# Kernel tuning notes

Measured on AMD Instinct MI355X. Metric: run time of the kernel, lower is better.

Reference implementation:

```python
import jax, jax.numpy as jnp
import numpy as np

N_EMBD = 1024
N_HEAD = 16
HEAD_SIZE = N_EMBD // N_HEAD


def setup_inputs() -> dict:
    key = jax.random.key(0)
    k_x, k_w, k_b = jax.random.split(key, 3)
    B, T, C = 2, 2048, N_EMBD
    x = jax.random.normal(k_x, (B, T, C), dtype=jnp.float32)
    # Linear(n_embd, 3*n_embd): weight [C, 3C] (applied as x @ W), bias [3C]
    w_qkv = jax.random.normal(k_w, (C, 3 * C), dtype=jnp.float32) * (1.0 / np.sqrt(C))
    b_qkv = jax.random.normal(k_b, (3 * C,), dtype=jnp.float32) * 0.02
    return {"x": x, "w_qkv": w_qkv, "b_qkv": b_qkv}


def reference(x, w_qkv, b_qkv):
    B, T, C = x.shape
    H, D = N_HEAD, HEAD_SIZE
    qkv = x @ w_qkv + b_qkv                      # [B, T, 3C]
    q, k, v = jnp.split(qkv, 3, axis=-1)         # each [B, T, C]
    # [B, T, C] -> [B, H, T, D]
    q = q.reshape(B, T, H, D).transpose(0, 2, 1, 3)
    k = k.reshape(B, T, H, D).transpose(0, 2, 1, 3)
    v = v.reshape(B, T, H, D).transpose(0, 2, 1, 3)
    scores = jnp.einsum('bhqd,bhkd->bhqk', q, k) / jnp.sqrt(jnp.float32(D))
    causal = jnp.tril(jnp.ones((T, T), dtype=bool))  # allow j <= i
    scores = jnp.where(causal[None, None, :, :], scores, -jnp.inf)
    weights = jax.nn.softmax(scores, axis=-1)    # [B, H, T, T]
    out = jnp.einsum('bhqk,bhkd->bhqd', weights, v)
    out = out.transpose(0, 2, 1, 3).reshape(B, T, C)
    return out
```

## Files before the change

kernel.cpp:

```cpp
#include <hip/hip_runtime.h>
#include <hip/hip_bf16.h>


#define CDIM  1024
#define C3    3072
#define HS    64
#define TLEN  2048
#define KVT   128
#define KSTR  72
#define VSTR  136
#define SCL   0.1803368801111204f

typedef __attribute__((ext_vector_type(8))) short bf16x8;
typedef __attribute__((ext_vector_type(4))) float f32x4;
typedef __attribute__((ext_vector_type(4))) unsigned short u16x4;

__device__ __forceinline__ unsigned short f2b(float f) {
    unsigned u = __float_as_uint(f);
    unsigned r = (u + 0x7FFFu + ((u >> 16) & 1u)) >> 16;
    return (unsigned short)r;
}
__device__ __forceinline__ float b2f(unsigned short u) {
    return __uint_as_float(((unsigned)u) << 16);
}
__device__ __forceinline__ float fexp2(float x) {
    return __builtin_amdgcn_exp2f(x);
}
__device__ __forceinline__ unsigned pkbf(float a, float b) {
    float2 f; f.x = a; f.y = b;
    __hip_bfloat162 h = __float22bfloat162_rn(f);
    union { __hip_bfloat162 h2; unsigned u; } c;
    c.h2 = h;
    return c.u;
}
__device__ __forceinline__ void gl_lds16(const unsigned short* g, unsigned short* l) {
    __builtin_amdgcn_global_load_lds((const __attribute__((address_space(1))) void*)g,
                                     (__attribute__((address_space(3))) void*)l, 16, 0, 0);
}
__device__ __forceinline__ int detect_bf(const void* bias, int lane) {
    unsigned w = ((const unsigned*)bias)[lane];
    unsigned e = (w >> 7) & 0xFF;
    unsigned long long m = __ballot(e >= 100 && e <= 135);
    return __popcll(m) >= 48;
}

__device__ __forceinline__ void plswap(unsigned x, unsigned& y0, unsigned& y1) {
    unsigned aa = x, bb = x;
    asm("v_permlane32_swap_b32 %0, %1" : "+v"(aa), "+v"(bb));
    asm("v_permlane16_swap_b32 %0, %1" : "+v"(aa), "+v"(bb));
    y0 = aa; y1 = bb;
}
__device__ __forceinline__ bf16x8 xfrag(unsigned x00, unsigned x01,
                                        unsigned x10, unsigned x11, int qsel) {
    unsigned y000, y100, y001, y101, y010, y110, y011, y111;
    plswap(x00, y000, y100);
    plswap(x01, y001, y101);
    plswap(x10, y010, y110);
    plswap(x11, y011, y111);
    union { unsigned u[4]; bf16x8 v; } r;
    r.u[0] = qsel ? y010 : y000;
    r.u[1] = qsel ? y011 : y001;
    r.u[2] = qsel ? y110 : y100;
    r.u[3] = qsel ? y111 : y101;
    return r.v;
}

__global__ __launch_bounds__(256) void k_prep(const void* __restrict__ w,
                                              const void* __restrict__ x,
                                              const void* __restrict__ bias,
                                              unsigned short* __restrict__ wt,
                                              unsigned short* __restrict__ xb) {
    __shared__ unsigned short tile[64 * 66];
    int t = threadIdx.x;
    int isbf = detect_bf(bias, t & 63);
    int bid = blockIdx.x;

    if (bid < 768) {
        int n0 = (bid % 48) * 64;
        int k0 = (bid / 48) * 64;
        for (int i = 0; i < 16; ++i) {
            int idx = t + i * 256;
            int r = idx >> 6, c = idx & 63;
            unsigned short v;
            if (isbf) v = ((const unsigned short*)w)[(k0 + r) * C3 + n0 + c];
            else      v = f2b(((const float*)w)[(k0 + r) * C3 + n0 + c]);
            tile[r * 66 + c] = v;
        }
        __syncthreads();
        for (int i = 0; i < 16; ++i) {
            int idx = t + i * 256;
            int r = idx >> 6, c = idx & 63;
            wt[(n0 + r) * CDIM + k0 + c] = tile[c * 66 + r];
        }
    }
    if (!isbf) {
        const float* s = (const float*)x;
        unsigned* d = (unsigned*)xb;
        int base = bid * 1024;
        for (int j = t; j < 1024; j += 256) {
            int idx = base + j;
            float a = s[2 * idx], b = s[2 * idx + 1];
            d[idx] = (unsigned)f2b(a) | ((unsigned)f2b(b) << 16);
        }
    }
}

__global__ __launch_bounds__(256, 3) void k_gemm_qkv(const void* __restrict__ xraw,
                                                     const unsigned short* __restrict__ xb,
                                                     const void* __restrict__ biasraw,
                                                     const unsigned short* __restrict__ Bt,
                                                     unsigned short* __restrict__ qk,
                                                     unsigned short* __restrict__ vtg) {
    __shared__ __align__(16) unsigned short As[128 * 64];
    __shared__ __align__(16) unsigned short Bs[128 * 64];
    int tid  = threadIdx.x;
    int lane = tid & 63, wv = tid >> 6;
    int quad = lane >> 4, l16 = lane & 15;
    int isbf = detect_bf(biasraw, lane);
    const unsigned short* A = isbf ? (const unsigned short*)xraw : xb;

    int m0 = blockIdx.y * 128, n0 = blockIdx.x * 128;
    int wm = (wv >> 1) * 64, wn = (wv & 1) * 64;

    f32x4 acc[4][4] = {};

    int srow = wv * 8 + (lane >> 3);
    int kcg8 = (((lane & 7) ^ (lane >> 3)) * 8);
    const unsigned short* Ag = A  + (m0 + srow) * CDIM + kcg8;
    const unsigned short* Bg = Bt + (n0 + srow) * CDIM + kcg8;
    unsigned short* lA = &As[srow * 64 + (lane & 7) * 8];
    unsigned short* lB = &Bs[srow * 64 + (lane & 7) * 8];

    for (int k0 = 0; k0 < CDIM; k0 += 64) {
        __syncthreads();
        for (int j = 0; j < 4; ++j) {
            gl_lds16(Ag + j * (32 * CDIM), lA + j * (32 * 64));
            gl_lds16(Bg + j * (32 * CDIM), lB + j * (32 * 64));
        }
        Ag += 64; Bg += 64;
        __syncthreads();

        for (int kk = 0; kk < 2; ++kk) {
            int sw = (l16 & 7);
            bf16x8 af[4], bfr[4];
            for (int mt = 0; mt < 4; ++mt)
                af[mt] = *(const bf16x8*)&As[(wm + mt * 16 + l16) * 64 + (((kk * 4 + quad) ^ sw) * 8)];
            for (int nt = 0; nt < 4; ++nt)
                bfr[nt] = *(const bf16x8*)&Bs[(wn + nt * 16 + l16) * 64 + (((kk * 4 + quad) ^ sw) * 8)];
            for (int mt = 0; mt < 4; ++mt)
                for (int nt = 0; nt < 4; ++nt)
                    acc[mt][nt] = __builtin_amdgcn_mfma_f32_16x16x32_bf16(af[mt], bfr[nt], acc[mt][nt], 0, 0, 0);
        }
    }

    if (n0 < 2048) {
        for (int mt = 0; mt < 4; ++mt) {
            int row = m0 + wm + mt * 16 + quad * 4;
            for (int nt = 0; nt < 4; ++nt) {
                int col = n0 + wn + nt * 16 + l16;
                float bv = isbf ? b2f(((const unsigned short*)biasraw)[col])
                                : ((const float*)biasraw)[col];
                for (int i = 0; i < 4; ++i)
                    qk[(row + i) * 2048 + col] = f2b(acc[mt][nt][i] + bv);
            }
        }
    } else {
        for (int mt = 0; mt < 4; ++mt) {
            int row = m0 + wm + mt * 16 + quad * 4;
            int t = row & 2047, b = row >> 11;
            for (int nt = 0; nt < 4; ++nt) {
                int col = n0 + wn + nt * 16 + l16;
                float bv = isbf ? b2f(((const unsigned short*)biasraw)[col])
                                : ((const float*)biasraw)[col];
                int hh = (col - 2048) >> 6, d = (col - 2048) & 63;
                u16x4 pk;
                for (int i = 0; i < 4; ++i) pk[i] = f2b(acc[mt][nt][i] + bv);
                *(u16x4*)&vtg[((b * 16 + hh) * 64 + d) * TLEN + t] = pk;
            }
        }
    }
}

__global__ __launch_bounds__(512, 4) void k_attn(const unsigned short* __restrict__ qk,
                                                 const unsigned short* __restrict__ vtg,
                                                 const void* __restrict__ biasraw,
                                                 void* __restrict__ outv) {
    __shared__ __align__(16) unsigned short Ks[2][128 * KSTR];
    __shared__ __align__(16) unsigned short Vt[2][64 * VSTR];

    int tid  = threadIdx.x;
    int lane = tid & 63, wv = tid >> 6;
    int quad = lane >> 4, l16 = lane & 15;
    int isbf = detect_bf(biasraw, lane);
    int bh = blockIdx.x;
    int y  = blockIdx.y;
    int jj = (y < 8) ? (15 - 2 * y) : (2 * (y - 8));
    int b = bh >> 4, h = bh & 15;
    int rowbase = b * TLEN;

    int qt = 8 * jj + wv;
    int q0 = qt * 16;
    int T  = jj + 1;

    bf16x8 qf[2];
    for (int kh = 0; kh < 2; ++kh)
        qf[kh] = *(const bf16x8*)&qk[(rowbase + q0 + l16) * 2048 + h * HS + kh * 32 + quad * 8];

    f32x4 o[4] = {};
    float ls = 0.f;

    int krow = tid >> 3;
    int kc8  = (tid & 7) * 8;
    int vrow = tid >> 4;
    int vc8  = (tid & 15) * 8;
    const unsigned short* kgB = qk  + (rowbase + krow) * 2048 + CDIM + h * HS + kc8;
    const unsigned short* vgB = vtg + (bh * 64 + vrow) * TLEN + vc8;

    {
        uint4 k0 = *(const uint4*)kgB;
        uint4 k1 = *(const uint4*)(kgB + 64 * 2048);
        uint4 v0 = *(const uint4*)vgB;
        uint4 v1 = *(const uint4*)(vgB + 32 * TLEN);
        *(uint4*)&Ks[0][krow * KSTR + kc8]        = k0;
        *(uint4*)&Ks[0][(krow + 64) * KSTR + kc8] = k1;
        *(uint4*)&Vt[0][vrow * VSTR + vc8]        = v0;
        *(uint4*)&Vt[0][(vrow + 32) * VSTR + vc8] = v1;
    }
    __syncthreads();

    for (int t = 0; t < T; ++t) {
        int cur = t & 1;
        const unsigned short* KsC = Ks[cur];
        const unsigned short* VtC = Vt[cur];
        int kv0 = t * KVT;

        uint4 kn0, kn1, vn0, vn1;
        bool pf = (t + 1 < T);
        if (pf) {
            const unsigned short* kg = kgB + (t + 1) * KVT * 2048;
            const unsigned short* vg = vgB + (t + 1) * KVT;
            kn0 = *(const uint4*)kg;
            kn1 = *(const uint4*)(kg + 64 * 2048);
            vn0 = *(const uint4*)vg;
            vn1 = *(const uint4*)(vg + 32 * TLEN);
        }

        f32x4 s[8];
        #pragma unroll
        for (int nt = 0; nt < 8; ++nt) {
            bf16x8 kf0 = *(const bf16x8*)&KsC[(nt * 16 + l16) * KSTR + quad * 8];
            bf16x8 kf1 = *(const bf16x8*)&KsC[(nt * 16 + l16) * KSTR + 32 + quad * 8];
            f32x4 z = {};
            z = __builtin_amdgcn_mfma_f32_16x16x32_bf16(kf0, qf[0], z, 0, 0, 0);
            z = __builtin_amdgcn_mfma_f32_16x16x32_bf16(kf1, qf[1], z, 0, 0, 0);
            s[nt] = z;
        }

        unsigned sp[8][2];
        float psum = 0.f;
        if (t == T - 1) {
            int q = q0 + l16;
            #pragma unroll
            for (int nt = 0; nt < 8; ++nt) {
                float p[4];
                #pragma unroll
                for (int i = 0; i < 4; ++i) {
                    float arg = fminf(fmaf(s[nt][i], SCL, -12.0f), 30.0f);
                    int kv = kv0 + nt * 16 + quad * 4 + i;
                    if (kv > q) arg = -1e30f;
                    p[i] = fexp2(arg);
                    psum += p[i];
                }
                sp[nt][0] = pkbf(p[0], p[1]);
                sp[nt][1] = pkbf(p[2], p[3]);
            }
        } else {
            #pragma unroll
            for (int nt = 0; nt < 8; ++nt) {
                float p[4];
                #pragma unroll
                for (int i = 0; i < 4; ++i) {
                    float arg = fminf(fmaf(s[nt][i], SCL, -12.0f), 30.0f);
                    p[i] = fexp2(arg);
                    psum += p[i];
                }
                sp[nt][0] = pkbf(p[0], p[1]);
                sp[nt][1] = pkbf(p[2], p[3]);
            }
        }
        ls += psum;

        if (pf) {
            int nxt = cur ^ 1;
            *(uint4*)&Ks[nxt][krow * KSTR + kc8]        = kn0;
            *(uint4*)&Ks[nxt][(krow + 64) * KSTR + kc8] = kn1;
            *(uint4*)&Vt[nxt][vrow * VSTR + vc8]        = vn0;
            *(uint4*)&Vt[nxt][(vrow + 32) * VSTR + vc8] = vn1;
        }

        int qsel = quad & 2;
        #pragma unroll
        for (int kq = 0; kq < 4; ++kq) {
            bf16x8 fB = xfrag(sp[2 * kq][0], sp[2 * kq][1],
                              sp[2 * kq + 1][0], sp[2 * kq + 1][1], qsel);
            __builtin_amdgcn_s_setprio(1);
            #pragma unroll
            for (int dt = 0; dt < 4; ++dt) {
                bf16x8 av = *(const bf16x8*)&VtC[(dt * 16 + l16) * VSTR + kq * 32 + quad * 8];
                o[dt] = __builtin_amdgcn_mfma_f32_16x16x32_bf16(av, fB, o[dt], 0, 0, 0);
            }
            __builtin_amdgcn_s_setprio(0);
        }

        __syncthreads();
    }

    {
        float l = ls;
        l += __shfl_xor(l, 16);
        l += __shfl_xor(l, 32);
        float inv = 1.0f / l;
        int q = q0 + l16;
        if (isbf) {
            unsigned short* out = (unsigned short*)outv;
            for (int dt = 0; dt < 4; ++dt) {
                u16x4 ov;
                for (int i = 0; i < 4; ++i) ov[i] = f2b(o[dt][i] * inv);
                *(u16x4*)&out[(rowbase + q) * CDIM + h * HS + dt * 16 + quad * 4] = ov;
            }
        } else {
            float* out = (float*)outv;
            for (int dt = 0; dt < 4; ++dt) {
                float4 ov;
                ov.x = o[dt][0] * inv; ov.y = o[dt][1] * inv;
                ov.z = o[dt][2] * inv; ov.w = o[dt][3] * inv;
                *(float4*)&out[(rowbase + q) * CDIM + h * HS + dt * 16 + quad * 4] = ov;
            }
        }
    }
}

extern "C" void kernel_launch(void* const* d_in, const int* in_sizes, int n_in,
                              void* d_out, int out_size, void* d_ws, size_t ws_size,
                              hipStream_t stream) {
    const void* x    = d_in[0];
    const void* w    = d_in[1];
    const void* bias = d_in[2];

    char* ws = (char*)d_ws;
    unsigned short* xb  = (unsigned short*)ws;
    unsigned short* wt  = (unsigned short*)(ws + (8u  << 20));
    unsigned short* qk  = (unsigned short*)(ws + (16u << 20));
    unsigned short* vtg = (unsigned short*)(ws + (32u << 20));

    k_prep<<<2048, 256, 0, stream>>>(w, x, bias, wt, xb);
    k_gemm_qkv<<<dim3(24, 32), 256, 0, stream>>>(x, xb, bias, wt, qk, vtg);
    k_attn<<<dim3(32, 16), 512, 0, stream>>>(qk, vtg, bias, d_out);
}
```

Measured before the change: 162.9 us.

## Restructure attention into 64-query blocks with split-KV warps and LDS merge

The attention kernel now uses 256-thread blocks, each covering 64 query rows with 64-row KV tiles, and the grid doubles to 32x32. The four warps form two query pairs: each warp handles 32 queries against half of every KV tile, and the partial outputs and row sums are combined through shared memory at the end. The aim is finer-grained blocks for better load balance and occupancy, with causal masking applied only on the diagonal tile and fully masked half-tiles skipped. In exchange there are more KV tile iterations with a barrier each, a merge step, and some warps sitting idle on the final tile.

```diff
diff --git a/kernel.cpp b/kernel.cpp
--- a/kernel.cpp
+++ b/kernel.cpp
@@ -6,9 +6,9 @@
 #define C3    3072
 #define HS    64
 #define TLEN  2048
-#define KVT   128
+#define KVT   64
 #define KSTR  72
-#define VSTR  136
+#define VSTR  72
 #define SCL   0.1803368801111204f
 
 typedef __attribute__((ext_vector_type(8))) short bf16x8;
@@ -181,11 +181,11 @@
     }
 }
 
-__global__ __launch_bounds__(512, 4) void k_attn(const unsigned short* __restrict__ qk,
+__global__ __launch_bounds__(256, 4) void k_attn(const unsigned short* __restrict__ qk,
                                                  const unsigned short* __restrict__ vtg,
                                                  const void* __restrict__ biasraw,
                                                  void* __restrict__ outv) {
-    __shared__ __align__(16) unsigned short Ks[2][128 * KSTR];
+    __shared__ __align__(16) unsigned short Ks[2][64 * KSTR];
     __shared__ __align__(16) unsigned short Vt[2][64 * VSTR];
 
     int tid  = threadIdx.x;
@@ -193,38 +193,38 @@
     int quad = lane >> 4, l16 = lane & 15;
     int isbf = detect_bf(biasraw, lane);
     int bh = blockIdx.x;
-    int y  = blockIdx.y;
-    int jj = (y < 8) ? (15 - 2 * y) : (2 * (y - 8));
+    int g  = 31 - blockIdx.y;
     int b = bh >> 4, h = bh & 15;
     int rowbase = b * TLEN;
 
-    int qt = 8 * jj + wv;
-    int q0 = qt * 16;
-    int T  = jj + 1;
-
-    bf16x8 qf[2];
-    for (int kh = 0; kh < 2; ++kh)
-        qf[kh] = *(const bf16x8*)&qk[(rowbase + q0 + l16) * 2048 + h * HS + kh * 32 + quad * 8];
-
-    f32x4 o[4] = {};
-    float ls = 0.f;
-
-    int krow = tid >> 3;
-    int kc8  = (tid & 7) * 8;
-    int vrow = tid >> 4;
-    int vc8  = (tid & 15) * 8;
-    const unsigned short* kgB = qk  + (rowbase + krow) * 2048 + CDIM + h * HS + kc8;
-    const unsigned short* vgB = vtg + (bh * 64 + vrow) * TLEN + vc8;
+    int s_ = wv >> 1;
+    int p  = wv & 1;
+    int qbase = 64 * g + 32 * s_;
+    int T = g + 1;
+
+    bf16x8 qf[2][2];
+    for (int qt = 0; qt < 2; ++qt)
+        for (int kh = 0; kh < 2; ++kh)
+            qf[qt][kh] = *(const bf16x8*)&qk[(rowbase + qbase + qt * 16 + l16) * 2048
+                                            + h * HS + kh * 32 + quad * 8];
+
+    f32x4 o[2][4] = {};
+    float ls[2] = {0.f, 0.f};
+
+    int srow = tid >> 2;
+    int sc   = (tid & 3) * 8;
+    const unsigned short* kgB = qk  + (rowbase + srow) * 2048 + CDIM + h * HS + sc;
+    const unsigned short* vgB = vtg + (bh * 64 + srow) * TLEN + sc;
 
     {
         uint4 k0 = *(const uint4*)kgB;
-        uint4 k1 = *(const uint4*)(kgB + 64 * 2048);
+        uint4 k1 = *(const uint4*)(kgB + 32);
         uint4 v0 = *(const uint4*)vgB;
-        uint4 v1 = *(const uint4*)(vgB + 32 * TLEN);
-        *(uint4*)&Ks[0][krow * KSTR + kc8]        = k0;
-        *(uint4*)&Ks[0][(krow + 64) * KSTR + kc8] = k1;
-        *(uint4*)&Vt[0][vrow * VSTR + vc8]        = v0;
-        *(uint4*)&Vt[0][(vrow + 32) * VSTR + vc8] = v1;
+        uint4 v1 = *(const uint4*)(vgB + 32);
+        *(uint4*)&Ks[0][srow * KSTR + sc]      = k0;
+        *(uint4*)&Ks[0][srow * KSTR + sc + 32] = k1;
+        *(uint4*)&Vt[0][srow * VSTR + sc]      = v0;
+        *(uint4*)&Vt[0][srow * VSTR + sc + 32] = v1;
     }
     __syncthreads();
 
@@ -233,6 +233,8 @@
         const unsigned short* KsC = Ks[cur];
         const unsigned short* VtC = Vt[cur];
         int kv0 = t * KVT;
+        bool act = (p == 0) || (s_ == 1) || (t < T - 1);
+        bool dm  = (t == T - 1) && (p == s_);
 
         uint4 kn0, kn1, vn0, vn1;
         bool pf = (t + 1 < T);
@@ -240,101 +242,129 @@
             const unsigned short* kg = kgB + (t + 1) * KVT * 2048;
             const unsigned short* vg = vgB + (t + 1) * KVT;
             kn0 = *(const uint4*)kg;
-            kn1 = *(const uint4*)(kg + 64 * 2048);
+            kn1 = *(const uint4*)(kg + 32);
             vn0 = *(const uint4*)vg;
-            vn1 = *(const uint4*)(vg + 32 * TLEN);
-        }
-
-        f32x4 s[8];
-        #pragma unroll
-        for (int nt = 0; nt < 8; ++nt) {
-            bf16x8 kf0 = *(const bf16x8*)&KsC[(nt * 16 + l16) * KSTR + quad * 8];
-            bf16x8 kf1 = *(const bf16x8*)&KsC[(nt * 16 + l16) * KSTR + 32 + quad * 8];
-            f32x4 z = {};
-            z = __builtin_amdgcn_mfma_f32_16x16x32_bf16(kf0, qf[0], z, 0, 0, 0);
-            z = __builtin_amdgcn_mfma_f32_16x16x32_bf16(kf1, qf[1], z, 0, 0, 0);
-            s[nt] = z;
-        }
-
-        unsigned sp[8][2];
-        float psum = 0.f;
-        if (t == T - 1) {
-            int q = q0 + l16;
-            #pragma unroll
-            for (int nt = 0; nt < 8; ++nt) {
-                float p[4];
+            vn1 = *(const uint4*)(vg + 32);
+        }
+
+        unsigned sp[2][2][2];
+        if (act) {
+            bf16x8 kf[2][2];
+            #pragma unroll
+            for (int nt = 0; nt < 2; ++nt) {
+                const unsigned short* kb = &KsC[(32 * p + nt * 16 + l16) * KSTR + quad * 8];
+                kf[nt][0] = *(const bf16x8*)kb;
+                kf[nt][1] = *(const bf16x8*)(kb + 32);
+            }
+            f32x4 sv[2][2];
+            __builtin_amdgcn_s_setprio(1);
+            #pragma unroll
+            for (int qt = 0; qt < 2; ++qt)
                 #pragma unroll
-                for (int i = 0; i < 4; ++i) {
-                    float arg = fminf(fmaf(s[nt][i], SCL, -12.0f), 30.0f);
-                    int kv = kv0 + nt * 16 + quad * 4 + i;
-                    if (kv > q) arg = -1e30f;
-                    p[i] = fexp2(arg);
-                    psum += p[i];
+                for (int nt = 0; nt < 2; ++nt) {
+                    f32x4 z = {};
+                    z = __builtin_amdgcn_mfma_f32_16x16x32_bf16(kf[nt][0], qf[qt][0], z, 0, 0, 0);
+                    z = __builtin_amdgcn_mfma_f32_16x16x32_bf16(kf[nt][1], qf[qt][1], z, 0, 0, 0);
+                    sv[qt][nt] = z;
                 }
-                sp[nt][0] = pkbf(p[0], p[1]);
-                sp[nt][1] = pkbf(p[2], p[3]);
-            }
-        } else {
-            #pragma unroll
-            for (int nt = 0; nt < 8; ++nt) {
-                float p[4];
+            __builtin_amdgcn_s_setprio(0);
+            #pragma unroll
+            for (int qt = 0; qt < 2; ++qt) {
+                float psum = 0.f;
+                int q = qbase + qt * 16 + l16;
                 #pragma unroll
-                for (int i = 0; i < 4; ++i) {
-                    float arg = fminf(fmaf(s[nt][i], SCL, -12.0f), 30.0f);
-                    p[i] = fexp2(arg);
-                    psum += p[i];
+                for (int nt = 0; nt < 2; ++nt) {
+                    float pv[4];
+                    #pragma unroll
+                    for (int i = 0; i < 4; ++i) {
+                        float arg = fminf(fmaf(sv[qt][nt][i], SCL, -12.0f), 30.0f);
+                        if (dm) {
+                            int kv = kv0 + 32 * p + nt * 16 + quad * 4 + i;
+                            if (kv > q) arg = -1e30f;
+                        }
+                        pv[i] = fexp2(arg);
+                        psum += pv[i];
+                    }
+                    sp[qt][nt][0] = pkbf(pv[0], pv[1]);
+                    sp[qt][nt][1] = pkbf(pv[2], pv[3]);
                 }
-                sp[nt][0] = pkbf(p[0], p[1]);
-                sp[nt][1] = pkbf(p[2], p[3]);
-            }
-        }
-        ls += psum;
+                ls[qt] += psum;
+            }
+        }
 
         if (pf) {
             int nxt = cur ^ 1;
-            *(uint4*)&Ks[nxt][krow * KSTR + kc8]        = kn0;
-            *(uint4*)&Ks[nxt][(krow + 64) * KSTR + kc8] = kn1;
-            *(uint4*)&Vt[nxt][vrow * VSTR + vc8]        = vn0;
-            *(uint4*)&Vt[nxt][(vrow + 32) * VSTR + vc8] = vn1;
-        }
-
-        int qsel = quad & 2;
+            *(uint4*)&Ks[nxt][srow * KSTR + sc]      = kn0;
+            *(uint4*)&Ks[nxt][srow * KSTR + sc + 32] = kn1;
+            *(uint4*)&Vt[nxt][srow * VSTR + sc]      = vn0;
+            *(uint4*)&Vt[nxt][srow * VSTR + sc + 32] = vn1;
+        }
+
+        if (act) {
+            int qsel = quad & 2;
+            bf16x8 f0 = xfrag(sp[0][0][0], sp[0][0][1], sp[0][1][0], sp[0][1][1], qsel);
+            bf16x8 f1 = xfrag(sp[1][0][0], sp[1][0][1], sp[1][1][0], sp[1][1][1], qsel);
+            __builtin_amdgcn_s_setprio(1);
+            #pragma unroll
+            for (int dt = 0; dt < 4; ++dt) {
+                bf16x8 av = *(const bf16x8*)&VtC[(dt * 16 + l16) * VSTR + 32 * p + quad * 8];
+                o[0][dt] = __builtin_amdgcn_mfma_f32_16x16x32_bf16(av, f0, o[0][dt], 0, 0, 0);
+                o[1][dt] = __builtin_amdgcn_mfma_f32_16x16x32_bf16(av, f1, o[1][dt], 0, 0, 0);
+            }
+            __builtin_amdgcn_s_setprio(0);
+        }
+
+        __syncthreads();
+    }
+
+    #pragma unroll
+    for (int qt = 0; qt < 2; ++qt) {
+        ls[qt] += __shfl_xor(ls[qt], 16);
+        ls[qt] += __shfl_xor(ls[qt], 32);
+    }
+    float* mrg  = (float*)&Ks[0][0];
+    float* lbuf = (float*)&Vt[0][0];
+
+    if (p == 1) {
         #pragma unroll
-        for (int kq = 0; kq < 4; ++kq) {
-            bf16x8 fB = xfrag(sp[2 * kq][0], sp[2 * kq][1],
-                              sp[2 * kq + 1][0], sp[2 * kq + 1][1], qsel);
-            __builtin_amdgcn_s_setprio(1);
-            #pragma unroll
-            for (int dt = 0; dt < 4; ++dt) {
-                bf16x8 av = *(const bf16x8*)&VtC[(dt * 16 + l16) * VSTR + kq * 32 + quad * 8];
-                o[dt] = __builtin_amdgcn_mfma_f32_16x16x32_bf16(av, fB, o[dt], 0, 0, 0);
-            }
-            __builtin_amdgcn_s_setprio(0);
-        }
-
-        __syncthreads();
-    }
-
-    {
-        float l = ls;
-        l += __shfl_xor(l, 16);
-        l += __shfl_xor(l, 32);
-        float inv = 1.0f / l;
-        int q = q0 + l16;
-        if (isbf) {
-            unsigned short* out = (unsigned short*)outv;
-            for (int dt = 0; dt < 4; ++dt) {
-                u16x4 ov;
-                for (int i = 0; i < 4; ++i) ov[i] = f2b(o[dt][i] * inv);
-                *(u16x4*)&out[(rowbase + q) * CDIM + h * HS + dt * 16 + quad * 4] = ov;
-            }
-        } else {
-            float* out = (float*)outv;
-            for (int dt = 0; dt < 4; ++dt) {
-                float4 ov;
-                ov.x = o[dt][0] * inv; ov.y = o[dt][1] * inv;
-                ov.z = o[dt][2] * inv; ov.w = o[dt][3] * inv;
-                *(float4*)&out[(rowbase + q) * CDIM + h * HS + dt * 16 + quad * 4] = ov;
+        for (int qt = 0; qt < 2; ++qt)
+            #pragma unroll
+            for (int dt = 0; dt < 4; ++dt)
+                *(f32x4*)&mrg[s_ * (32 * 68) + (qt * 16 + l16) * 68 + dt * 16 + quad * 4] = o[qt][dt];
+        if (quad == 0) {
+            lbuf[s_ * 32 + l16]      = ls[0];
+            lbuf[s_ * 32 + 16 + l16] = ls[1];
+        }
+    }
+    __syncthreads();
+    if (p == 0) {
+        #pragma unroll
+        for (int qt = 0; qt < 2; ++qt) {
+            float lt = ls[qt] + lbuf[s_ * 32 + qt * 16 + l16];
+            float inv = 1.0f / lt;
+            int q = qbase + qt * 16 + l16;
+            if (isbf) {
+                unsigned short* out = (unsigned short*)outv;
+                #pragma unroll
+                for (int dt = 0; dt < 4; ++dt) {
+                    f32x4 m = *(const f32x4*)&mrg[s_ * (32 * 68) + (qt * 16 + l16) * 68 + dt * 16 + quad * 4];
+                    u16x4 ov;
+                    #pragma unroll
+                    for (int i = 0; i < 4; ++i) ov[i] = f2b((o[qt][dt][i] + m[i]) * inv);
+                    *(u16x4*)&out[(rowbase + q) * CDIM + h * HS + dt * 16 + quad * 4] = ov;
+                }
+            } else {
+                float* out = (float*)outv;
+                #pragma unroll
+                for (int dt = 0; dt < 4; ++dt) {
+                    f32x4 m = *(const f32x4*)&mrg[s_ * (32 * 68) + (qt * 16 + l16) * 68 + dt * 16 + quad * 4];
+                    float4 ov;
+                    ov.x = (o[qt][dt][0] + m[0]) * inv;
+                    ov.y = (o[qt][dt][1] + m[1]) * inv;
+                    ov.z = (o[qt][dt][2] + m[2]) * inv;
+                    ov.w = (o[qt][dt][3] + m[3]) * inv;
+                    *(float4*)&out[(rowbase + q) * CDIM + h * HS + dt * 16 + quad * 4] = ov;
+                }
             }
         }
     }
@@ -355,5 +385,5 @@
 
     k_prep<<<2048, 256, 0, stream>>>(w, x, bias, wt, xb);
     k_gemm_qkv<<<dim3(24, 32), 256, 0, stream>>>(x, xb, bias, wt, qk, vtg);
-    k_attn<<<dim3(32, 16), 512, 0, stream>>>(qk, vtg, bias, d_out);
-}
+    k_attn<<<dim3(32, 32), 256, 0, stream>>>(qk, vtg, bias, d_out);
+}
```

Result: faster. 151.0 us (-7.3%).
